# Performance work log

Measured on AMD Instinct MI355X. Metric: run time of the kernel, lower is better.

## Reference

```python
import jax, jax.numpy as jnp
import numpy as np

B, L, D, N, KEEP, HID = 64, 256, 128, 8192, 64, 1024
IN_DIM = D + KEEP * D + 1  # q + packed subset keys + log_count


def setup_inputs() -> dict:
    key = jax.random.key(0)
    ks = jax.random.split(key, 7)
    q = jax.random.normal(ks[0], (N, D), jnp.float32)
    k = jax.random.normal(ks[1], (B, L, D), jnp.float32)
    batch_idx = jax.random.randint(ks[2], (N,), 0, B)
    mask = jax.random.randint(ks[3], (N, L), 0, 2).astype(bool)
    count = jax.random.randint(ks[4], (N,), 0, L)
    W1 = jax.random.normal(ks[5], (IN_DIM, HID), jnp.float32) / np.sqrt(IN_DIM).astype(np.float32)
    b1 = jnp.zeros((HID,), jnp.float32)
    W2 = jax.random.normal(ks[6], (HID, 1), jnp.float32) / np.sqrt(HID).astype(np.float32)
    b2 = jnp.zeros((1,), jnp.float32)
    return dict(q=q, k=k, batch_idx=batch_idx, mask=mask, count=count,
                W1=W1, b1=b1, W2=W2, b2=b2)


def _pack_subset_keys(k, batch_idx, mask):
    # chain_k: [N, L, D] gather of per-chain key blocks
    chain_k = k[batch_idx]
    pos = jnp.arange(L, dtype=jnp.float32)
    # score = L - pos for masked positions, 0 otherwise -> topk picks first KEEP masked positions
    scores = mask.astype(jnp.float32) * (jnp.float32(L) - pos)[None, :]
    top_scores, top_idx = jax.lax.top_k(scores, KEEP)
    picked = top_scores > 0
    sortable = jnp.where(picked, top_idx, L)  # sentinel L for unpicked
    sortable = jnp.sort(sortable, axis=1)     # restore ascending position order
    picked = sortable < L
    safe_idx = jnp.where(picked, sortable, 0)
    packed = jnp.take_along_axis(chain_k, safe_idx[:, :, None], axis=1)  # [N, KEEP, D]
    packed = packed * picked[:, :, None].astype(packed.dtype)
    return packed.reshape(N, KEEP * D)


def reference(q, k, batch_idx, mask, count, W1, b1, W2, b2):
    packed = _pack_subset_keys(k, batch_idx, mask)
    log_count = jnp.log1p(count.astype(q.dtype))[:, None]
    feat = jnp.concatenate([q, packed, log_count], axis=-1)  # [N, IN_DIM]
    h = jax.nn.gelu(feat @ W1 + b1, approximate=False)       # torch GELU = exact erf
    return (h @ W2 + b2).squeeze(-1)                          # [N]
```

## Files before the change

kernel.cpp:

```cpp
#include <hip/hip_runtime.h>
#include <math.h>

#define N_ROWS 8192
#define B_CH   64
#define L_SEQ  256
#define D_DIM  128
#define KEEP   64
#define HID    1024
#define KTOT   8320
#define KTILES 260
#define HTILES 64

#define KOFF   (N_ROWS * D_DIM)
#define ZOFF   (KOFF + B_CH * L_SEQ * D_DIM)
#define BUF_ELEMS (ZOFF + 128)

#define PACK_BLOCKS 256
#define QK_BLOCKS   1537
#define W1T_BLOCKS  2080
#define PREP_GRID   (PACK_BLOCKS + QK_BLOCKS + W1T_BLOCKS)

typedef unsigned short ushort_t;
typedef __attribute__((ext_vector_type(8))) short  short8;
typedef __attribute__((ext_vector_type(4))) float  float4v;

__device__ __forceinline__ ushort_t f2bf(float f) {
    union { float f; unsigned int u; } v; v.f = f;
    unsigned int u = v.u;
    unsigned int r = u + 0x7fffu + ((u >> 16) & 1u);
    return (ushort_t)(r >> 16);
}

__device__ __forceinline__ void glds16(const void* g, void* l) {
    __builtin_amdgcn_global_load_lds(
        (const __attribute__((address_space(1))) unsigned int*)g,
        (__attribute__((address_space(3))) unsigned int*)l,
        16, 0, 0);
}

__global__ void prep(const float* __restrict__ q, const float* __restrict__ k,
                     const float* __restrict__ W1, const int* __restrict__ mask,
                     const int* __restrict__ batch_idx, const int* __restrict__ count,
                     const float* __restrict__ b2,
                     ushort_t* __restrict__ buf, ushort_t* __restrict__ w1f,
                     int* __restrict__ srcLUT, float* __restrict__ logc,
                     float* __restrict__ out) {
    __shared__ __align__(16) char smem[16640];
    const int blk = blockIdx.x;
    const int t = threadIdx.x;

    if (blk < PACK_BLOCKS) {
        const int n0 = blk * 32;
        int* sidx = (int*)smem;
        int* bidx_l = (int*)(smem + 32 * 65 * 4);
        for (int i = t; i < 32 * 65; i += 256) sidx[i] = -1;
        if (t < 32) {
            int n = n0 + t;
            bidx_l[t] = batch_idx[n];
            logc[n] = log1pf((float)count[n]);
            srcLUT[n] = n * D_DIM;
            out[n] = b2[0];
        }
        __syncthreads();
        const int w = t >> 6, l = t & 63;
        const unsigned long long ltm = (1ull << l) - 1ull;
        for (int r = 0; r < 8; ++r) {
            const int lr = w * 8 + r;
            const int* mrow = mask + (size_t)(n0 + lr) * L_SEQ;
            int m0 = mrow[l] != 0;
            int m1 = mrow[64 + l] != 0;
            int m2 = mrow[128 + l] != 0;
            int m3 = mrow[192 + l] != 0;
            unsigned long long b0 = __ballot(m0), b1 = __ballot(m1);
            unsigned long long b2v = __ballot(m2), b3 = __ballot(m3);
            int p1 = (int)__popcll(b0);
            int p2 = p1 + (int)__popcll(b1);
            int p3 = p2 + (int)__popcll(b2v);
            int* row = sidx + lr * 65;
            if (m0) { int rk = (int)__popcll(b0 & ltm);       if (rk < KEEP) row[rk] = l; }
            if (m1) { int rk = p1 + (int)__popcll(b1 & ltm);  if (rk < KEEP) row[rk] = 64 + l; }
            if (m2) { int rk = p2 + (int)__popcll(b2v & ltm); if (rk < KEEP) row[rk] = 128 + l; }
            if (m3) { int rk = p3 + (int)__popcll(b3 & ltm);  if (rk < KEEP) row[rk] = 192 + l; }
        }
        __syncthreads();
        for (int e = t; e < KEEP * 32; e += 256) {
            int j = e >> 5, nl = e & 31;
            int s = sidx[nl * 65 + j];
            srcLUT[(size_t)(j + 1) * N_ROWS + n0 + nl] =
                (s >= 0) ? (KOFF + (bidx_l[nl] * L_SEQ + s) * D_DIM) : ZOFF;
        }

    } else if (blk < PACK_BLOCKS + QK_BLOCKS) {
        int c = (blk - PACK_BLOCKS) * 256 + t;
        if (c >= BUF_ELEMS / 8) return;
        int e = c * 8;
        float4 x0, x1;
        if (e < KOFF) {
            const float4* s = (const float4*)(q + e);
            x0 = s[0]; x1 = s[1];
        } else if (e < ZOFF) {
            const float4* s = (const float4*)(k + (e - KOFF));
            x0 = s[0]; x1 = s[1];
        } else {
            x0 = make_float4(0.f, 0.f, 0.f, 0.f);
            x1 = x0;
        }
        union { ushort_t s[8]; uint4 v; } o;
        o.s[0] = f2bf(x0.x); o.s[1] = f2bf(x0.y); o.s[2] = f2bf(x0.z); o.s[3] = f2bf(x0.w);
        o.s[4] = f2bf(x1.x); o.s[5] = f2bf(x1.y); o.s[6] = f2bf(x1.z); o.s[7] = f2bf(x1.w);
        *(uint4*)(buf + e) = o.v;

    } else {
        const int idx = blk - (PACK_BLOCKS + QK_BLOCKS);
        const int k0 = (idx % 130) * 64, h0 = (idx / 130) * 64;
        float (*tile)[65] = (float(*)[65])smem;
        const int hl = t & 63, kl = t >> 6;
#pragma unroll
        for (int i = 0; i < 16; ++i) {
            int kk = kl + i * 4;
            tile[kk][hl] = W1[(size_t)(k0 + kk) * HID + h0 + hl];
        }
        __syncthreads();
#pragma unroll
        for (int i = 0; i < 2; ++i) {
            int s = i * 256 + t;
            int c = s >> 6, l = s & 63;
            int qt = c >> 2, ht = c & 3;
            int ln = l & 15, quad = l >> 4;
            union { ushort_t sv[8]; uint4 v; } o;
#pragma unroll
            for (int j = 0; j < 8; ++j)
                o.sv[j] = f2bf(tile[qt * 32 + quad * 8 + j][ht * 16 + ln]);
            size_t dst = (((size_t)(h0 / 16 + ht) * KTILES + (k0 / 32 + qt)) * 64 + l) * 8;
            *(uint4*)(w1f + dst) = o.v;
        }
    }
}

__global__ __launch_bounds__(256, 2)
void gemm_mlp(const ushort_t* __restrict__ buf, const ushort_t* __restrict__ w1f,
              const int* __restrict__ srcLUT, const float* __restrict__ logc,
              const float* __restrict__ W1, const float* __restrict__ b1,
              const float* __restrict__ W2, float* __restrict__ out) {
    __shared__ ushort_t As[128 * 128];

    const int t = threadIdx.x;
    const int blkH = blockIdx.x, blkM = blockIdx.y;
    const int wave = t >> 6, lane = t & 63;
    const int wm = wave >> 1, wh = wave & 1;
    const int ln = lane & 15, quad = lane >> 4;

    float4v acc[4][4];
#pragma unroll
    for (int i = 0; i < 4; ++i)
#pragma unroll
        for (int j = 0; j < 4; ++j)
#pragma unroll
            for (int r = 0; r < 4; ++r) acc[i][j][r] = 0.0f;

    const int tr = t >> 4;
    const int pg = (t & 15) ^ tr;
    ushort_t* lA = As + t * 8;
    const int* lutBase = srcLUT + blkM * 128 + tr;

    const ushort_t* bp[4];
#pragma unroll
    for (int ni = 0; ni < 4; ++ni)
        bp[ni] = w1f + ((size_t)(blkH * 8 + wh * 4 + ni) * KTILES * 64 + lane) * 8;

    int offA[8];
#pragma unroll
    for (int i = 0; i < 8; ++i) offA[i] = lutBase[i * 16];

    for (int bi = 0; bi < 65; ++bi) {
#pragma unroll
        for (int i = 0; i < 8; ++i)
            glds16(buf + offA[i] + pg * 8, lA + i * 2048);
        short8 bq[4][4];
#pragma unroll
        for (int kk = 0; kk < 4; ++kk)
#pragma unroll
            for (int ni = 0; ni < 4; ++ni)
                bq[kk][ni] = *(const short8*)(bp[ni] + (size_t)(bi * 4 + kk) * 512);
        int offN[8];
        if (bi < 64) {
#pragma unroll
            for (int i = 0; i < 8; ++i) offN[i] = lutBase[(bi + 1) * N_ROWS + i * 16];
        }
        __syncthreads();
#pragma unroll
        for (int kk = 0; kk < 4; ++kk) {
            short8 af[4];
#pragma unroll
            for (int mi = 0; mi < 4; ++mi) {
                const int row = wm * 64 + mi * 16 + ln;
                const int sl = (kk * 4 + quad) ^ ln;
                af[mi] = *(const short8*)(As + row * 128 + sl * 8);
            }
#pragma unroll
            for (int mi = 0; mi < 4; ++mi)
#pragma unroll
                for (int ni = 0; ni < 4; ++ni)
                    acc[mi][ni] = __builtin_amdgcn_mfma_f32_16x16x32_bf16(
                        af[mi], bq[kk][ni], acc[mi][ni], 0, 0, 0);
        }
        __syncthreads();
#pragma unroll
        for (int i = 0; i < 8; ++i) offA[i] = offN[i];
    }

    const float* w1last = W1 + (size_t)KTOT * HID;
    float w1l[4], b1v[4], w2v[4];
#pragma unroll
    for (int ni = 0; ni < 4; ++ni) {
        int h = blkH * 128 + wh * 64 + ni * 16 + ln;
        w1l[ni] = w1last[h];
        b1v[ni] = b1[h];
        w2v[ni] = W2[h];
    }
    const int nbase = blkM * 128 + wm * 64 + quad * 4;
#pragma unroll
    for (int mi = 0; mi < 4; ++mi) {
#pragma unroll
        for (int rg = 0; rg < 4; ++rg) {
            const int n = nbase + mi * 16 + rg;
            const float lc = logc[n];
            float s = 0.0f;
#pragma unroll
            for (int ni = 0; ni < 4; ++ni) {
                float pre = acc[mi][ni][rg] + lc * w1l[ni] + b1v[ni];
                float hv = 0.5f * pre * (1.0f + erff(pre * 0.70710678118654752f));
                s += hv * w2v[ni];
            }
            s += __shfl_xor(s, 1);
            s += __shfl_xor(s, 2);
            s += __shfl_xor(s, 4);
            s += __shfl_xor(s, 8);
            if (ln == 0) atomicAdd(out + n, s);
        }
    }
}

extern "C" void kernel_launch(void* const* d_in, const int* in_sizes, int n_in,
                              void* d_out, int out_size, void* d_ws, size_t ws_size,
                              hipStream_t stream) {
    const float* q     = (const float*)d_in[0];
    const float* k     = (const float*)d_in[1];
    const int*   bidx  = (const int*)d_in[2];
    const int*   mask  = (const int*)d_in[3];
    const int*   count = (const int*)d_in[4];
    const float* W1    = (const float*)d_in[5];
    const float* b1    = (const float*)d_in[6];
    const float* W2    = (const float*)d_in[7];
    const float* b2    = (const float*)d_in[8];
    float* out = (float*)d_out;

    char* ws = (char*)d_ws;
    ushort_t* buf    = (ushort_t*)(ws);
    ushort_t* w1f    = (ushort_t*)(ws + 6291712);
    int*      srcLUT = (int*)(ws + 6291712 + 17039360);
    float*    logc   = (float*)(ws + 6291712 + 17039360 + 2129920);

    prep<<<PREP_GRID, 256, 0, stream>>>(q, k, W1, mask, bidx, count, b2,
                                        buf, w1f, srcLUT, logc, out);
    gemm_mlp<<<dim3(HID / 128, N_ROWS / 128), 256, 0, stream>>>(
        buf, w1f, srcLUT, logc, W1, b1, W2, out);
}
```

Before: 241.4 us.

## Double-buffer A tiles in LDS with explicit vmcnt waits and barriers in GEMM

Splits the 128x128 A LDS tile into two 64-wide halves and ping-pongs between them. Global-to-LDS loads for the next half are issued before the MFMAs on the current half, and B fragments are prefetched one half-step ahead. Explicit s_waitcnt, sched_barrier, s_barrier and setprio calls replace __syncthreads, aiming to overlap memory latency with compute. The W1 transpose in the prep kernel also switches to float4 loads. The manual vmcnt counting is fragile and could race if the number of loads in flight differs from what it assumes.

```diff
diff --git a/kernel.cpp b/kernel.cpp
--- a/kernel.cpp
+++ b/kernel.cpp
@@ -37,6 +37,9 @@
         (__attribute__((address_space(3))) unsigned int*)l,
         16, 0, 0);
 }
+
+#define SCHED0() __builtin_amdgcn_sched_barrier(0)
+#define WAITVM(n) do { asm volatile("s_waitcnt vmcnt(" #n ")" ::: "memory"); SCHED0(); } while (0)
 
 __global__ void prep(const float* __restrict__ q, const float* __restrict__ k,
                      const float* __restrict__ W1, const int* __restrict__ mask,
@@ -114,11 +117,13 @@
         const int idx = blk - (PACK_BLOCKS + QK_BLOCKS);
         const int k0 = (idx % 130) * 64, h0 = (idx / 130) * 64;
         float (*tile)[65] = (float(*)[65])smem;
-        const int hl = t & 63, kl = t >> 6;
-#pragma unroll
-        for (int i = 0; i < 16; ++i) {
-            int kk = kl + i * 4;
-            tile[kk][hl] = W1[(size_t)(k0 + kk) * HID + h0 + hl];
+        const int r0 = t >> 4, c4 = (t & 15) * 4;
+#pragma unroll
+        for (int i = 0; i < 4; ++i) {
+            const int r = r0 + i * 16;
+            const float4 v = *(const float4*)(W1 + (size_t)(k0 + r) * HID + h0 + c4);
+            tile[r][c4 + 0] = v.x; tile[r][c4 + 1] = v.y;
+            tile[r][c4 + 2] = v.z; tile[r][c4 + 3] = v.w;
         }
         __syncthreads();
 #pragma unroll
@@ -142,7 +147,8 @@
               const int* __restrict__ srcLUT, const float* __restrict__ logc,
               const float* __restrict__ W1, const float* __restrict__ b1,
               const float* __restrict__ W2, float* __restrict__ out) {
-    __shared__ ushort_t As[128 * 128];
+    __shared__ __align__(16) ushort_t As0[128 * 64];
+    __shared__ __align__(16) ushort_t As1[128 * 64];
 
     const int t = threadIdx.x;
     const int blkH = blockIdx.x, blkM = blockIdx.y;
@@ -158,56 +164,119 @@
 #pragma unroll
             for (int r = 0; r < 4; ++r) acc[i][j][r] = 0.0f;
 
-    const int tr = t >> 4;
-    const int pg = (t & 15) ^ tr;
-    ushort_t* lA = As + t * 8;
-    const int* lutBase = srcLUT + blkM * 128 + tr;
-
-    const ushort_t* bp[4];
-#pragma unroll
-    for (int ni = 0; ni < 4; ++ni)
-        bp[ni] = w1f + ((size_t)(blkH * 8 + wh * 4 + ni) * KTILES * 64 + lane) * 8;
-
-    int offA[8];
-#pragma unroll
-    for (int i = 0; i < 8; ++i) offA[i] = lutBase[i * 16];
-
-    for (int bi = 0; bi < 65; ++bi) {
-#pragma unroll
-        for (int i = 0; i < 8; ++i)
-            glds16(buf + offA[i] + pg * 8, lA + i * 2048);
-        short8 bq[4][4];
-#pragma unroll
-        for (int kk = 0; kk < 4; ++kk)
-#pragma unroll
-            for (int ni = 0; ni < 4; ++ni)
-                bq[kk][ni] = *(const short8*)(bp[ni] + (size_t)(bi * 4 + kk) * 512);
-        int offN[8];
-        if (bi < 64) {
-#pragma unroll
-            for (int i = 0; i < 8; ++i) offN[i] = lutBase[(bi + 1) * N_ROWS + i * 16];
-        }
-        __syncthreads();
-#pragma unroll
-        for (int kk = 0; kk < 4; ++kk) {
+    const int swz = (t & 7) ^ ((t >> 3) & 7);
+    const ushort_t* bufc = buf + swz * 8;
+    ushort_t* lA0 = As0 + t * 8;
+    ushort_t* lA1 = As1 + t * 8;
+    const int* lutRow = srcLUT + blkM * 128 + (t >> 3);
+
+    const ushort_t* bpA[4];
+    const ushort_t* bpB[4];
+#pragma unroll
+    for (int ni = 0; ni < 4; ++ni) {
+        bpA[ni] = w1f + ((size_t)(blkH * 8 + wh * 4 + ni) * KTILES * 64 + lane) * 8;
+        bpB[ni] = bpA[ni] + 2048;
+    }
+
+    const int rowB = (wm * 64 + ln) * 64;
+    const int sl0 = ((quad) ^ (ln & 7)) * 8;
+    const int sl1 = ((4 + quad) ^ (ln & 7)) * 8;
+
+    short8 bqE[2][4], bqO[2][4];
+    int off0, off1, off2, off3;
+    int offN0, offN1, offN2, offN3;
+
+    off0 = lutRow[0];  off1 = lutRow[32];
+    off2 = lutRow[64]; off3 = lutRow[96];
+    glds16(bufc + off0, lA0);
+    glds16(bufc + off1, lA0 + 2048);
+    glds16(bufc + off2, lA0 + 4096);
+    glds16(bufc + off3, lA0 + 6144);
+#pragma unroll
+    for (int ni = 0; ni < 4; ++ni) {
+        bqE[0][ni] = *(const short8*)(bpA[ni]);
+        bqE[1][ni] = *(const short8*)(bpA[ni] + 512);
+    }
+
+    for (int m = 0; m < 65; ++m) {
+        const int* lutP = lutRow + (size_t)((m < 64) ? (m + 1) : 64) * N_ROWS;
+
+#pragma unroll
+        for (int ni = 0; ni < 4; ++ni) {
+            bqO[0][ni] = *(const short8*)(bpA[ni] + 1024);
+            bqO[1][ni] = *(const short8*)(bpA[ni] + 1536);
+        }
+        SCHED0();
+        WAITVM(8);
+        glds16(bufc + off0 + 64, lA1);
+        glds16(bufc + off1 + 64, lA1 + 2048);
+        glds16(bufc + off2 + 64, lA1 + 4096);
+        glds16(bufc + off3 + 64, lA1 + 6144);
+        offN0 = lutP[0];  offN1 = lutP[32];
+        offN2 = lutP[64]; offN3 = lutP[96];
+        SCHED0();
+        __builtin_amdgcn_s_barrier();
+        SCHED0();
+        __builtin_amdgcn_s_setprio(1);
+#pragma unroll
+        for (int kk = 0; kk < 2; ++kk) {
             short8 af[4];
-#pragma unroll
-            for (int mi = 0; mi < 4; ++mi) {
-                const int row = wm * 64 + mi * 16 + ln;
-                const int sl = (kk * 4 + quad) ^ ln;
-                af[mi] = *(const short8*)(As + row * 128 + sl * 8);
-            }
+            const int slk = kk ? sl1 : sl0;
+#pragma unroll
+            for (int mi = 0; mi < 4; ++mi)
+                af[mi] = *(const short8*)(As0 + rowB + mi * 1024 + slk);
 #pragma unroll
             for (int mi = 0; mi < 4; ++mi)
 #pragma unroll
                 for (int ni = 0; ni < 4; ++ni)
                     acc[mi][ni] = __builtin_amdgcn_mfma_f32_16x16x32_bf16(
-                        af[mi], bq[kk][ni], acc[mi][ni], 0, 0, 0);
-        }
-        __syncthreads();
-#pragma unroll
-        for (int i = 0; i < 8; ++i) offA[i] = offN[i];
-    }
+                        af[mi], bqE[kk][ni], acc[mi][ni], 0, 0, 0);
+        }
+        __builtin_amdgcn_s_setprio(0);
+        SCHED0();
+        __builtin_amdgcn_s_barrier();
+        SCHED0();
+
+#pragma unroll
+        for (int ni = 0; ni < 4; ++ni) {
+            const ushort_t* pB = (m < 64) ? bpB[ni] : bpA[ni];
+            bqE[0][ni] = *(const short8*)(pB);
+            bqE[1][ni] = *(const short8*)(pB + 512);
+        }
+        SCHED0();
+        WAITVM(8);
+        glds16(bufc + offN0, lA0);
+        glds16(bufc + offN1, lA0 + 2048);
+        glds16(bufc + offN2, lA0 + 4096);
+        glds16(bufc + offN3, lA0 + 6144);
+        SCHED0();
+        __builtin_amdgcn_s_barrier();
+        SCHED0();
+        __builtin_amdgcn_s_setprio(1);
+#pragma unroll
+        for (int kk = 0; kk < 2; ++kk) {
+            short8 af[4];
+            const int slk = kk ? sl1 : sl0;
+#pragma unroll
+            for (int mi = 0; mi < 4; ++mi)
+                af[mi] = *(const short8*)(As1 + rowB + mi * 1024 + slk);
+#pragma unroll
+            for (int mi = 0; mi < 4; ++mi)
+#pragma unroll
+                for (int ni = 0; ni < 4; ++ni)
+                    acc[mi][ni] = __builtin_amdgcn_mfma_f32_16x16x32_bf16(
+                        af[mi], bqO[kk][ni], acc[mi][ni], 0, 0, 0);
+        }
+        __builtin_amdgcn_s_setprio(0);
+        SCHED0();
+        __builtin_amdgcn_s_barrier();
+        SCHED0();
+
+        off0 = offN0; off1 = offN1; off2 = offN2; off3 = offN3;
+#pragma unroll
+        for (int ni = 0; ni < 4; ++ni) { bpA[ni] += 2048; bpB[ni] += 2048; }
+    }
+    WAITVM(0);
 
     const float* w1last = W1 + (size_t)KTOT * HID;
     float w1l[4], b1v[4], w2v[4];
```

After: 266.3 us. 10.3% more time.
